# Optimization experiments

Measured on AMD Instinct MI355X. Metric: run time of the kernel, lower is better.

## Reference

```python
import jax, jax.numpy as jnp
import numpy as np

B, N, DS, DP, H, DH, DFF = 1, 1024, 768, 128, 16, 48, 1536


def _ln(x, eps=1e-5):
    m = jnp.mean(x, axis=-1, keepdims=True)
    v = jnp.var(x, axis=-1, keepdims=True)
    return (x - m) * jax.lax.rsqrt(v + eps)


def _ada_ln(a, s, gw, gb, bw):
    # AF3-style adaptive layernorm: sigmoid(Linear(LN(s))) * LN(a) + Linear(LN(s))
    sn = _ln(s)
    return jax.nn.sigmoid(sn @ gw + gb) * _ln(a) + sn @ bw


def setup_inputs() -> dict:
    key = jax.random.key(0)
    ks = jax.random.split(key, 24)
    w = lambda k, shape: jax.random.normal(k, shape, dtype=jnp.float32) * 0.02
    return {
        'x': jax.random.normal(ks[0], (B, N, DS), dtype=jnp.float32),
        'single_cond': jax.random.normal(ks[1], (B, N, DS), dtype=jnp.float32),
        'pair_cond': jax.random.normal(ks[2], (B, N, N, DP), dtype=jnp.float32),
        'attn_gamma_w': w(ks[3], (DS, DS)), 'attn_gamma_b': jnp.zeros((DS,), jnp.float32),
        'attn_beta_w': w(ks[4], (DS, DS)),
        'wq': w(ks[5], (DS, H * DH)), 'bq': jnp.zeros((H * DH,), jnp.float32),
        'wk': w(ks[6], (DS, H * DH)), 'wv': w(ks[7], (DS, H * DH)),
        'wb': w(ks[8], (DP, H)),
        'wg': w(ks[9], (DS, H * DH)),
        'wo': w(ks[10], (H * DH, DS)),
        'attn_gate_w': w(ks[11], (DS, DS)), 'attn_gate_b': jnp.full((DS,), -2.0, jnp.float32),
        'ff_gamma_w': w(ks[12], (DS, DS)), 'ff_gamma_b': jnp.zeros((DS,), jnp.float32),
        'ff_beta_w': w(ks[13], (DS, DS)),
        'ff_w1': w(ks[14], (DS, DFF)), 'ff_w2': w(ks[15], (DS, DFF)),
        'ff_w3': w(ks[16], (DFF, DS)),
        'ff_gate_w': w(ks[17], (DS, DS)), 'ff_gate_b': jnp.full((DS,), -2.0, jnp.float32),
        'mask': jnp.ones((B, N), dtype=bool),
    }


def reference(x, single_cond, pair_cond, attn_gamma_w, attn_gamma_b, attn_beta_w,
              wq, bq, wk, wv, wb, wg, wo, attn_gate_w, attn_gate_b,
              ff_gamma_w, ff_gamma_b, ff_beta_w, ff_w1, ff_w2, ff_w3,
              ff_gate_w, ff_gate_b, mask):
    # --- AttentionPairBias (edge bias + cond adaLN + gated output) ---
    a = _ada_ln(x, single_cond, attn_gamma_w, attn_gamma_b, attn_beta_w)
    q = (a @ wq + bq).reshape(B, N, H, DH)  # q has bias (q_use_bias=True)
    k = (a @ wk).reshape(B, N, H, DH)
    v = (a @ wv).reshape(B, N, H, DH)
    bias = jnp.einsum('bijp,ph->bhij', _ln(pair_cond), wb)  # pair bias per head
    logits = jnp.einsum('bihd,bjhd->bhij', q, k) * (1.0 / np.float32(np.sqrt(DH))) + bias
    logits = jnp.where(mask[:, None, None, :], logits, jnp.float32(-1e9))
    attn = jax.nn.softmax(logits, axis=-1)
    o = jnp.einsum('bhij,bjhd->bihd', attn, v)
    g = jax.nn.sigmoid(a @ wg).reshape(B, N, H, DH)  # gating (g_use_bias=False)
    attn_out = (g * o).reshape(B, N, H * DH) @ wo  # o_use_bias=False
    attn_out = jax.nn.sigmoid(single_cond @ attn_gate_w + attn_gate_b) * attn_out
    # --- ConditionedFeedForward (adaLN + SwiGLU + cond output gate) ---
    f = _ada_ln(x, single_cond, ff_gamma_w, ff_gamma_b, ff_beta_w)
    h = jax.nn.silu(f @ ff_w1) * (f @ ff_w2)
    ff_out = jax.nn.sigmoid(single_cond @ ff_gate_w + ff_gate_b) * (h @ ff_w3)
    # dropout p=0 (eval) -> identity; residual add of both branches
    return x + attn_out + ff_out
```

## Files before the change

### kernel.cpp

```cpp
#include <hip/hip_runtime.h>
#include <hip/hip_bf16.h>


typedef __attribute__((ext_vector_type(8))) short bf16x8;
typedef __attribute__((ext_vector_type(4))) float f32x4;
typedef __attribute__((ext_vector_type(4))) unsigned short us4;

#define DEVFN static __device__ __forceinline__

DEVFN float bf2f(unsigned short u){
  union { unsigned int u; float f; } v; v.u = ((unsigned int)u) << 16; return v.f;
}
DEVFN unsigned short f2bf(float f){
  union { float f; unsigned int u; } v; v.f = f;
  unsigned int r = v.u + 0x7fffu + ((v.u >> 16) & 1u);
  return (unsigned short)(r >> 16);
}
DEVFN float sigf(float x){ return 1.f / (1.f + __expf(-x)); }

DEVFN void gload16(const void* g, void* l){
  __builtin_amdgcn_global_load_lds(
      (const __attribute__((address_space(1))) void*)g,
      (__attribute__((address_space(3))) void*)l, 16, 0, 0);
}

#define OFF_SN    0x0000000ULL
#define OFF_SC    0x0180000ULL
#define OFF_XA    0x0300000ULL
#define OFF_W1    0x0600000ULL
#define OFF_W2    0x0A80000ULL
#define OFF_W3    0x0CC0000ULL
#define OFF_W4    0x1140000ULL
#define OFF_W5    0x15C0000ULL
#define OFF_W6    0x1800000ULL
#define OFF_BIAS1 0x1920000ULL
#define OFF_BIASG 0x1923000ULL
#define OFF_BIASQ 0x1924800ULL
#define OFF_G1    0x1930000ULL
#define OFF_GATES 0x2530000ULL
#define OFF_A     0x2B30000ULL
#define OFF_F     0x2CB0000ULL
#define OFF_QH    0x2E30000ULL
#define OFF_KH    0x2FB0000ULL
#define OFF_GH    0x3130000ULL
#define OFF_VT    0x3430000ULL
#define OFF_HH    0x4030000ULL
#define OFF_GO    0x4330000ULL
#define OFF_PB    0x47B0000ULL

struct WJobs {
  const float* src[14];
  unsigned long long dst[14];
  int K[14];
  int N[14];
  int rowmul[14];
  int rowoff[14];
};

__global__ __launch_bounds__(256) void prep_kernel(WJobs jobs, char* ws,
    const float* __restrict__ x, const float* __restrict__ sc,
    unsigned short* __restrict__ sn_bf, unsigned short* __restrict__ sc_bf,
    float* __restrict__ xa,
    const float* agb, const float* bq, const float* gtb, const float* fgtb,
    const float* fgb, float* bias1, float* biasg, float* biasq){
  const int bid = blockIdx.x;
  const int tid = threadIdx.x;
  if(bid < 9792){
    int t = bid, z = 0;
    while(true){
      int nt = (jobs.N[z] >> 5) * (jobs.K[z] >> 5);
      if(t < nt) break;
      t -= nt; z++;
    }
    const int nx = jobs.N[z] >> 5;
    const int n0 = (t % nx) << 5, k0 = (t / nx) << 5;
    const int K = jobs.K[z], N = jobs.N[z];
    __shared__ float tt[32][33];
    const int tx = tid & 31, ty = tid >> 5;
    const float* src = jobs.src[z];
    #pragma unroll
    for(int i=0;i<4;i++)
      tt[ty + i*8][tx] = src[(long long)(k0 + ty + i*8) * N + n0 + tx];
    __syncthreads();
    unsigned short* dst = (unsigned short*)(ws + jobs.dst[z]);
    const int rm = jobs.rowmul[z], ro = jobs.rowoff[z];
    #pragma unroll
    for(int i=0;i<4;i++)
      dst[(long long)((n0 + ty + i*8)*rm + ro) * K + k0 + tx] = f2bf(tt[tx][ty + i*8]);
    return;
  }
  if(bid >= 10816){
    int t = (bid - 10816) * 256 + tid;
    float v = 0.f;
    if(t < 768) v = agb[t];
    else if(t >= 1536 && t < 2304) v = fgb[t - 1536];
    bias1[t] = v;
    biasq[t] = (t < 768) ? bq[t] : 0.f;
    if(t < 1536) biasg[t] = (t < 768) ? gtb[t] : fgtb[t - 768];
    return;
  }
  const int row = bid - 9792;
  const float* xr = x + (long long)row * 768;
  const float* sr = sc + (long long)row * 768;
  float xs[3], ss[3];
  float s0=0.f, s1=0.f, s2=0.f, s3=0.f;
  #pragma unroll
  for(int i=0;i<3;i++){
    float xv = xr[tid + i*256], sv = sr[tid + i*256];
    xs[i]=xv; ss[i]=sv;
    s0 += xv; s1 += xv*xv; s2 += sv; s3 += sv*sv;
  }
  #pragma unroll
  for(int o=32;o;o>>=1){
    s0 += __shfl_xor(s0,o); s1 += __shfl_xor(s1,o);
    s2 += __shfl_xor(s2,o); s3 += __shfl_xor(s3,o);
  }
  __shared__ float red[4][4];
  const int w = tid >> 6;
  if((tid & 63) == 0){ red[0][w]=s0; red[1][w]=s1; red[2][w]=s2; red[3][w]=s3; }
  __syncthreads();
  float tx0 = red[0][0]+red[0][1]+red[0][2]+red[0][3];
  float tx1 = red[1][0]+red[1][1]+red[1][2]+red[1][3];
  float ts0 = red[2][0]+red[2][1]+red[2][2]+red[2][3];
  float ts1 = red[3][0]+red[3][1]+red[3][2]+red[3][3];
  const float inv = 1.f/768.f;
  float mx = tx0*inv, vx = tx1*inv - mx*mx;
  float ms = ts0*inv, vs = ts1*inv - ms*ms;
  float rsx = rsqrtf(vx + 1e-5f), rss = rsqrtf(vs + 1e-5f);
  #pragma unroll
  for(int i=0;i<3;i++){
    int c = tid + i*256;
    xa[(long long)row*768 + c]    = (xs[i]-mx)*rsx;
    sn_bf[(long long)row*768 + c] = f2bf((ss[i]-ms)*rss);
    sc_bf[(long long)row*768 + c] = f2bf(ss[i]);
  }
}

DEVFN void gemm_tile_f32(const unsigned short* __restrict__ A,
                         const unsigned short* __restrict__ Bt,
                         int N, int K, int m0, int n0,
                         const float* __restrict__ bias,
                         float* __restrict__ Cf, int epi,
                         unsigned short* sA, unsigned short* sB, int tid){
  const int w = tid >> 6, l = tid & 63, l15 = l & 15, l4 = l >> 4;
  const int wm = w >> 1, wn = w & 1;
  f32x4 zf = {0.f,0.f,0.f,0.f};
  f32x4 acc[4][4];
  #pragma unroll
  for(int m=0;m<4;m++)
    #pragma unroll
    for(int n=0;n<4;n++) acc[m][n] = zf;

  const int srow = w*16 + (l >> 2);
  const int scol = (l & 3) * 8;
  const unsigned short* gA = A  + (long long)(m0 + srow) * K + scol;
  const unsigned short* gB = Bt + (long long)(n0 + srow) * K + scol;
  unsigned short* lA0 = &sA[(w*16)*32];
  unsigned short* lA1 = &sA[(64 + w*16)*32];
  unsigned short* lB0 = &sB[(w*16)*32];
  unsigned short* lB1 = &sB[(64 + w*16)*32];
  const long long half = (long long)64 * K;

  for(int k0 = 0; k0 < K; k0 += 32){
    gload16(gA + k0, lA0);
    gload16(gA + half + k0, lA1);
    gload16(gB + k0, lB0);
    gload16(gB + half + k0, lB1);
    __syncthreads();
    bf16x8 af[4], bg[4];
    #pragma unroll
    for(int m=0;m<4;m++) af[m] = *(const bf16x8*)&sA[(wm*64 + m*16 + l15)*32 + l4*8];
    #pragma unroll
    for(int n=0;n<4;n++) bg[n] = *(const bf16x8*)&sB[(wn*64 + n*16 + l15)*32 + l4*8];
    #pragma unroll
    for(int m=0;m<4;m++)
      #pragma unroll
      for(int n=0;n<4;n++)
        acc[m][n] = __builtin_amdgcn_mfma_f32_16x16x32_bf16(af[m], bg[n], acc[m][n], 0, 0, 0);
    __syncthreads();
  }
  #pragma unroll
  for(int m=0;m<4;m++){
    #pragma unroll
    for(int n=0;n<4;n++){
      #pragma unroll
      for(int r=0;r<4;r++){
        const int i = m0 + wm*64 + m*16 + l4*4 + r;
        const int c = n0 + wn*64 + n*16 + l15;
        float v = acc[m][n][r] + bias[c];
        Cf[(long long)i*N + c] = epi ? sigf(v) : v;
      }
    }
  }
}

DEVFN void pair_block(int pbid, const float* __restrict__ pair,
                      const float* __restrict__ wb,
                      unsigned short* __restrict__ pb, int tid){
  const int l = tid & 63, w = tid >> 6, l15 = l & 15, l4 = l >> 4;
  bf16x8 wbf[4];
  #pragma unroll
  for(int c=0;c<4;c++){
    bf16x8 t;
    #pragma unroll
    for(int e=0;e<8;e++) t[e] = (short)f2bf(wb[(c*32 + l4*8 + e)*16 + l15]);
    wbf[c] = t;
  }
  f32x4 zf = {0.f,0.f,0.f,0.f};
  #pragma unroll
  for(int q=0;q<4;q++){
    const long long tile = (long long)pbid * 16 + q*4 + w;
    const long long row0 = tile << 4;
    const float* pr = pair + ((row0 + l15) << 7);
    float vals[32];
    #pragma unroll
    for(int c=0;c<4;c++){
      float4 v0 = *(const float4*)(pr + c*32 + l4*8);
      float4 v1 = *(const float4*)(pr + c*32 + l4*8 + 4);
      vals[c*8+0]=v0.x; vals[c*8+1]=v0.y; vals[c*8+2]=v0.z; vals[c*8+3]=v0.w;
      vals[c*8+4]=v1.x; vals[c*8+5]=v1.y; vals[c*8+6]=v1.z; vals[c*8+7]=v1.w;
    }
    float s=0.f, s2=0.f;
    #pragma unroll
    for(int e=0;e<32;e++){ s += vals[e]; s2 += vals[e]*vals[e]; }
    s += __shfl_xor(s, 16); s2 += __shfl_xor(s2, 16);
    s += __shfl_xor(s, 32); s2 += __shfl_xor(s2, 32);
    const float m = s * (1.f/128.f);
    const float rs = rsqrtf(s2*(1.f/128.f) - m*m + 1e-5f);
    f32x4 acc = zf;
    #pragma unroll
    for(int c=0;c<4;c++){
      bf16x8 af;
      #pragma unroll
      for(int e=0;e<8;e++) af[e] = (short)f2bf((vals[c*8+e] - m) * rs);
      acc = __builtin_amdgcn_mfma_f32_16x16x32_bf16(af, wbf[c], acc, 0,0,0);
    }
    us4 o;
    #pragma unroll
    for(int r=0;r<4;r++) o[r] = f2bf(acc[r]);
    *(us4*)&pb[((long long)l15 << 20) + row0 + l4*4] = o;
  }
}

__global__ __launch_bounds__(256) void fA_kernel(
    const float* __restrict__ pair, const float* __restrict__ wb,
    unsigned short* __restrict__ pb,
    const unsigned short* __restrict__ SN, const unsigned short* __restrict__ W1,
    const float* __restrict__ B1, float* __restrict__ G1,
    const unsigned short* __restrict__ SC, const unsigned short* __restrict__ W2,
    const float* __restrict__ BG, float* __restrict__ GT){
  __shared__ __align__(16) unsigned short sA[128*32];
  __shared__ __align__(16) unsigned short sB[128*32];
  const int bid = blockIdx.x;
  const int tid = threadIdx.x;
  if(bid < 288){
    if(bid < 192){
      gemm_tile_f32(SN, W1, 3072, 768, (bid & 7)*128, (bid >> 3)*128, B1, G1, 0, sA, sB, tid);
    } else {
      const int t = bid - 192;
      gemm_tile_f32(SC, W2, 1536, 768, (t & 7)*128, (t >> 3)*128, BG, GT, 1, sA, sB, tid);
    }
    return;
  }
  pair_block(bid - 288, pair, wb, pb, tid);
}

__global__ __launch_bounds__(256) void ew1_kernel(const float* __restrict__ g1,
    const float* __restrict__ xa, unsigned short* __restrict__ a_bf,
    unsigned short* __restrict__ f_bf, const float* __restrict__ x,
    float* __restrict__ out){
  const int i = blockIdx.x;
  const int c = blockIdx.y * 256 + threadIdx.x;
  const float* row = g1 + (long long)i * 3072;
  float xv = xa[(long long)i*768 + c];
  a_bf[(long long)i*768 + c] = f2bf(sigf(row[c])      * xv + row[768 + c]);
  f_bf[(long long)i*768 + c] = f2bf(sigf(row[1536+c]) * xv + row[2304 + c]);
  out[(long long)i*768 + c] = x[(long long)i*768 + c];
}

__global__ __launch_bounds__(256) void fB_kernel(
    const float* __restrict__ pair, const float* __restrict__ wb,
    unsigned short* __restrict__ pb,
    const unsigned short* __restrict__ A_, const unsigned short* __restrict__ W3,
    const float* __restrict__ BQ,
    unsigned short* __restrict__ QH, unsigned short* __restrict__ KH,
    unsigned short* __restrict__ GH, unsigned short* __restrict__ VT,
    const unsigned short* __restrict__ F_, const unsigned short* __restrict__ W4,
    unsigned short* __restrict__ HH){
  __shared__ __align__(16) unsigned short sA[128*32];
  __shared__ __align__(16) unsigned short sB[128*32];
  const int bid = blockIdx.x;
  const int tid = threadIdx.x;
  if(bid >= 384){
    pair_block(bid - 384 + 2048, pair, wb, pb, tid);
    return;
  }
  const bool isq = bid < 192;
  const int t = isq ? bid : bid - 192;
  const int m0 = (t & 7) * 128, n0 = (t >> 3) * 128;
  const unsigned short* A  = isq ? A_ : F_;
  const unsigned short* Bt = isq ? W3 : W4;
  const int K = 768;

  const int w = tid >> 6, l = tid & 63, l15 = l & 15, l4 = l >> 4;
  const int wm = w >> 1, wn = w & 1;
  f32x4 zf = {0.f,0.f,0.f,0.f};
  f32x4 acc[4][4];
  #pragma unroll
  for(int m=0;m<4;m++)
    #pragma unroll
    for(int n=0;n<4;n++) acc[m][n] = zf;

  const int srow = w*16 + (l >> 2);
  const int scol = (l & 3) * 8;
  const unsigned short* gA = A  + (long long)(m0 + srow) * K + scol;
  const unsigned short* gB = Bt + (long long)(n0 + srow) * K + scol;
  unsigned short* lA0 = &sA[(w*16)*32];
  unsigned short* lA1 = &sA[(64 + w*16)*32];
  unsigned short* lB0 = &sB[(w*16)*32];
  unsigned short* lB1 = &sB[(64 + w*16)*32];
  const long long half = (long long)64 * K;

  for(int k0 = 0; k0 < K; k0 += 32){
    gload16(gA + k0, lA0);
    gload16(gA + half + k0, lA1);
    gload16(gB + k0, lB0);
    gload16(gB + half + k0, lB1);
    __syncthreads();
    bf16x8 af[4], bg[4];
    #pragma unroll
    for(int m=0;m<4;m++) af[m] = *(const bf16x8*)&sA[(wm*64 + m*16 + l15)*32 + l4*8];
    #pragma unroll
    for(int n=0;n<4;n++) bg[n] = *(const bf16x8*)&sB[(wn*64 + n*16 + l15)*32 + l4*8];
    #pragma unroll
    for(int m=0;m<4;m++)
      #pragma unroll
      for(int n=0;n<4;n++)
        acc[m][n] = __builtin_amdgcn_mfma_f32_16x16x32_bf16(af[m], bg[n], acc[m][n], 0, 0, 0);
    __syncthreads();
  }
  if(isq){
    #pragma unroll
    for(int m=0;m<4;m++){
      #pragma unroll
      for(int n=0;n<4;n++){
        const int c = n0 + wn*64 + n*16 + l15;
        const int ibase = m0 + wm*64 + m*16 + l4*4;
        const int which = c / 768;
        const int h = (c % 768) / 48, d = c % 48;
        unsigned short vb[4];
        #pragma unroll
        for(int r=0;r<4;r++) vb[r] = f2bf(acc[m][n][r] + BQ[c]);
        if(which == 2){
          us4 o; o.x=vb[0]; o.y=vb[1]; o.z=vb[2]; o.w=vb[3];
          *(us4*)&VT[((long long)(c - 1536) << 10) + ibase] = o;
        } else {
          unsigned short* dst = (which == 0) ? QH : (which == 1) ? KH : GH;
          #pragma unroll
          for(int r=0;r<4;r++)
            dst[((long long)((h << 10) + ibase + r))*48 + d] = vb[r];
        }
      }
    }
  } else {
    #pragma unroll
    for(int m=0;m<4;m++){
      #pragma unroll
      for(int n=0;n<4;n++){
        #pragma unroll
        for(int r=0;r<4;r++){
          const int i = m0 + wm*64 + m*16 + l4*4 + r;
          const int c = n0 + wn*64 + n*16 + l15;
          float v = acc[m][n][r];
          float partner = __shfl_xor(v, 1);
          if((c & 1) == 0)
            HH[(long long)i*1536 + (c>>1)] = f2bf(v * sigf(v) * partner);
        }
      }
    }
  }
}

__global__ __launch_bounds__(256) void attn_kernel(
    const unsigned short* __restrict__ QH, const unsigned short* __restrict__ KH,
    const unsigned short* __restrict__ GH,
    const unsigned short* __restrict__ pbias,
    const unsigned short* __restrict__ VT,
    unsigned short* __restrict__ go){
  const int h  = blockIdx.x >> 6;
  const int i0 = (blockIdx.x & 63) << 4;
  const int tid = threadIdx.x;
  const int w = tid >> 6, l = tid & 63, l15 = l & 15, l4 = l >> 4;

  __shared__ unsigned short sP[16][1032];
  __shared__ float sRedM[16][4];
  __shared__ float sRedS[16][4];
  __shared__ float sO[4][16][48];

  f32x4 zf = {0.f,0.f,0.f,0.f};
  bf16x8 zero8 = {0,0,0,0,0,0,0,0};

  const unsigned short* pbh = pbias + ((long long)h << 20) + ((long long)i0 << 10);
  #pragma unroll
  for(int it=0; it<8; it++){
    const int idx = it*2048 + tid*8;
    const int r = idx >> 10, c = idx & 1023;
    *(bf16x8*)&sP[r][c] = *(const bf16x8*)&pbh[((long long)r << 10) + c];
  }

  f32x4 accs[16];
  #pragma unroll
  for(int f=0;f<16;f++) accs[f] = zf;
  bf16x8 aq0, aq1;
  {
    const unsigned short* qp = QH + (long long)((h << 10) + i0 + l15)*48;
    aq0 = *(const bf16x8*)(qp + l4*8);
    aq1 = *(const bf16x8*)(qp + 32 + l4*8);
  }
  const int jbase = w * 256;
  #pragma unroll
  for(int f=0; f<16; f++){
    const int j = jbase + f*16 + l15;
    const unsigned short* kp = KH + (long long)((h << 10) + j)*48;
    bf16x8 bk0 = *(const bf16x8*)(kp + l4*8);
    bf16x8 bk1 = *(const bf16x8*)(kp + 32 + l4*8);
    if(l4 >= 2) bk1 = zero8;
    accs[f] = __builtin_amdgcn_mfma_f32_16x16x32_bf16(aq0, bk0, accs[f], 0,0,0);
    accs[f] = __builtin_amdgcn_mfma_f32_16x16x32_bf16(aq1, bk1, accs[f], 0,0,0);
  }
  __syncthreads();

  const float scale = 0.14433756729740643f;
  #pragma unroll
  for(int f=0;f<16;f++){
    #pragma unroll
    for(int r=0;r<4;r++)
      accs[f][r] = accs[f][r]*scale + bf2f(sP[l4*4 + r][jbase + f*16 + l15]);
  }
  float pm[4];
  #pragma unroll
  for(int r=0;r<4;r++){
    float m = accs[0][r];
    #pragma unroll
    for(int f=1;f<16;f++) m = fmaxf(m, accs[f][r]);
    #pragma unroll
    for(int o=1;o<16;o<<=1) m = fmaxf(m, __shfl_xor(m, o));
    pm[r] = m;
  }
  if(l15 == 0){
    #pragma unroll
    for(int r=0;r<4;r++) sRedM[l4*4 + r][w] = pm[r];
  }
  __syncthreads();
  float rowm[4];
  #pragma unroll
  for(int r=0;r<4;r++){
    const int i = l4*4 + r;
    rowm[r] = fmaxf(fmaxf(sRedM[i][0], sRedM[i][1]), fmaxf(sRedM[i][2], sRedM[i][3]));
  }
  float psum[4] = {0.f,0.f,0.f,0.f};
  #pragma unroll
  for(int f=0;f<16;f++)
    #pragma unroll
    for(int r=0;r<4;r++){
      float p = __expf(accs[f][r] - rowm[r]);
      accs[f][r] = p;
      psum[r] += p;
    }
  #pragma unroll
  for(int r=0;r<4;r++)
    #pragma unroll
    for(int o=1;o<16;o<<=1) psum[r] += __shfl_xor(psum[r], o);
  if(l15 == 0){
    #pragma unroll
    for(int r=0;r<4;r++) sRedS[l4*4 + r][w] = psum[r];
  }
  #pragma unroll
  for(int f=0;f<16;f++)
    #pragma unroll
    for(int r=0;r<4;r++)
      sP[l4*4 + r][jbase + f*16 + l15] = f2bf(accs[f][r]);

  f32x4 acco[3];
  #pragma unroll
  for(int n=0;n<3;n++) acco[n] = zf;
  const unsigned short* vth = VT + ((long long)(h*48) << 10);
  #pragma unroll
  for(int c=0; c<4; c++){
    const int jb = jbase + c*64;
    #pragma unroll
    for(int kk=0; kk<2; kk++){
      bf16x8 pa = *(const bf16x8*)&sP[l15][jb + kk*32 + l4*8];
      #pragma unroll
      for(int n=0;n<3;n++){
        bf16x8 bv = *(const bf16x8*)&vth[((long long)(n*16 + l15) << 10) + jb + kk*32 + l4*8];
        acco[n] = __builtin_amdgcn_mfma_f32_16x16x32_bf16(pa, bv, acco[n], 0,0,0);
      }
    }
  }
  #pragma unroll
  for(int n=0;n<3;n++)
    #pragma unroll
    for(int r=0;r<4;r++)
      sO[w][l4*4 + r][n*16 + l15] = acco[n][r];
  __syncthreads();
  for(int t = tid; t < 768; t += 256){
    const int i = t / 48, d = t % 48;
    float o = sO[0][i][d] + sO[1][i][d] + sO[2][i][d] + sO[3][i][d];
    float lsum = sRedS[i][0] + sRedS[i][1] + sRedS[i][2] + sRedS[i][3];
    float gv = bf2f(GH[(long long)((h << 10) + i0 + i)*48 + d]);
    go[(long long)(i0 + i)*768 + h*48 + d] = f2bf(sigf(gv) * (o / lsum));
  }
}

__global__ __launch_bounds__(256) void final_kernel(
    const unsigned short* __restrict__ GO, const unsigned short* __restrict__ W6t,
    const unsigned short* __restrict__ HH, const unsigned short* __restrict__ W5t,
    const float* __restrict__ gates, float* __restrict__ out){
  __shared__ __align__(16) unsigned short sA[128*32];
  __shared__ __align__(16) unsigned short sB[128*32];
  const int m0 = blockIdx.x * 128, n0 = blockIdx.y * 128;
  const int z = blockIdx.z;
  const bool pA = z < 4;
  const unsigned short* A  = pA ? GO  : HH;
  const unsigned short* Bt = pA ? W6t : W5t;
  const int K    = pA ? 768 : 1536;
  const int kbeg = pA ? z*192 : (z-4)*384;
  const int kend = pA ? kbeg + 192 : kbeg + 384;
  const int goff = pA ? 0 : 768;
  const int tid = threadIdx.x;
  const int w = tid >> 6, l = tid & 63, l15 = l & 15, l4 = l >> 4;
  const int wm = w >> 1, wn = w & 1;
  f32x4 zf = {0.f,0.f,0.f,0.f};
  f32x4 acc[4][4];
  #pragma unroll
  for(int m=0;m<4;m++)
    #pragma unroll
    for(int n=0;n<4;n++) acc[m][n] = zf;

  const int srow = w*16 + (l >> 2);
  const int scol = (l & 3) * 8;
  const unsigned short* gA = A  + (long long)(m0 + srow) * K + scol;
  const unsigned short* gB = Bt + (long long)(n0 + srow) * K + scol;
  unsigned short* lA0 = &sA[(w*16)*32];
  unsigned short* lA1 = &sA[(64 + w*16)*32];
  unsigned short* lB0 = &sB[(w*16)*32];
  unsigned short* lB1 = &sB[(64 + w*16)*32];
  const long long half = (long long)64 * K;

  for(int k0 = kbeg; k0 < kend; k0 += 32){
    gload16(gA + k0, lA0);
    gload16(gA + half + k0, lA1);
    gload16(gB + k0, lB0);
    gload16(gB + half + k0, lB1);
    __syncthreads();
    bf16x8 af[4], bg[4];
    #pragma unroll
    for(int m=0;m<4;m++) af[m] = *(const bf16x8*)&sA[(wm*64 + m*16 + l15)*32 + l4*8];
    #pragma unroll
    for(int n=0;n<4;n++) bg[n] = *(const bf16x8*)&sB[(wn*64 + n*16 + l15)*32 + l4*8];
    #pragma unroll
    for(int m=0;m<4;m++)
      #pragma unroll
      for(int n=0;n<4;n++)
        acc[m][n] = __builtin_amdgcn_mfma_f32_16x16x32_bf16(af[m], bg[n], acc[m][n], 0, 0, 0);
    __syncthreads();
  }
  #pragma unroll
  for(int m=0;m<4;m++){
    #pragma unroll
    for(int n=0;n<4;n++){
      #pragma unroll
      for(int r=0;r<4;r++){
        const int i = m0 + wm*64 + m*16 + l4*4 + r;
        const int c = n0 + wn*64 + n*16 + l15;
        float v = gates[(long long)i*1536 + goff + c] * acc[m][n][r];
        __hip_atomic_fetch_add(&out[(long long)i*768 + c], v,
                               __ATOMIC_RELAXED, __HIP_MEMORY_SCOPE_AGENT);
      }
    }
  }
}

extern "C" void kernel_launch(void* const* d_in, const int* in_sizes, int n_in,
                              void* d_out, int out_size, void* d_ws, size_t ws_size,
                              hipStream_t stream){
  (void)in_sizes; (void)n_in; (void)out_size; (void)ws_size;
  const float* x    = (const float*)d_in[0];
  const float* sc   = (const float*)d_in[1];
  const float* pair = (const float*)d_in[2];
  const float* agw  = (const float*)d_in[3];
  const float* agb  = (const float*)d_in[4];
  const float* abw  = (const float*)d_in[5];
  const float* wq   = (const float*)d_in[6];
  const float* bq   = (const float*)d_in[7];
  const float* wk   = (const float*)d_in[8];
  const float* wv   = (const float*)d_in[9];
  const float* wb   = (const float*)d_in[10];
  const float* wg   = (const float*)d_in[11];
  const float* wo   = (const float*)d_in[12];
  const float* gtw  = (const float*)d_in[13];
  const float* gtb  = (const float*)d_in[14];
  const float* fgw  = (const float*)d_in[15];
  const float* fgb  = (const float*)d_in[16];
  const float* fbw  = (const float*)d_in[17];
  const float* fw1  = (const float*)d_in[18];
  const float* fw2  = (const float*)d_in[19];
  const float* fw3  = (const float*)d_in[20];
  const float* fgtw = (const float*)d_in[21];
  const float* fgtb = (const float*)d_in[22];
  float* out = (float*)d_out;
  char* ws = (char*)d_ws;

  unsigned short* SN   = (unsigned short*)(ws + OFF_SN);
  unsigned short* SC   = (unsigned short*)(ws + OFF_SC);
  float*          XA   = (float*)(ws + OFF_XA);
  unsigned short* W1   = (unsigned short*)(ws + OFF_W1);
  unsigned short* W2   = (unsigned short*)(ws + OFF_W2);
  unsigned short* W3   = (unsigned short*)(ws + OFF_W3);
  unsigned short* W4   = (unsigned short*)(ws + OFF_W4);
  unsigned short* W5   = (unsigned short*)(ws + OFF_W5);
  unsigned short* W6   = (unsigned short*)(ws + OFF_W6);
  float*          B1   = (float*)(ws + OFF_BIAS1);
  float*          BG   = (float*)(ws + OFF_BIASG);
  float*          BQ   = (float*)(ws + OFF_BIASQ);
  float*          G1   = (float*)(ws + OFF_G1);
  float*          GT   = (float*)(ws + OFF_GATES);
  unsigned short* A_   = (unsigned short*)(ws + OFF_A);
  unsigned short* F_   = (unsigned short*)(ws + OFF_F);
  unsigned short* QH   = (unsigned short*)(ws + OFF_QH);
  unsigned short* KH   = (unsigned short*)(ws + OFF_KH);
  unsigned short* GH   = (unsigned short*)(ws + OFF_GH);
  unsigned short* VT   = (unsigned short*)(ws + OFF_VT);
  unsigned short* HH   = (unsigned short*)(ws + OFF_HH);
  unsigned short* GO   = (unsigned short*)(ws + OFF_GO);
  unsigned short* PB   = (unsigned short*)(ws + OFF_PB);

  WJobs jobs;
  int ji = 0;
  auto setj = [&](const float* s, unsigned long long off, int K, int N,
                  int rm = 1, int ro = 0){
    jobs.src[ji]=s; jobs.dst[ji]=off; jobs.K[ji]=K; jobs.N[ji]=N;
    jobs.rowmul[ji]=rm; jobs.rowoff[ji]=ro; ji++;
  };
  const unsigned long long W768 = 768ULL*768ULL*2ULL;
  setj(agw,  OFF_W1 + 0*W768, 768, 768);
  setj(abw,  OFF_W1 + 1*W768, 768, 768);
  setj(fgw,  OFF_W1 + 2*W768, 768, 768);
  setj(fbw,  OFF_W1 + 3*W768, 768, 768);
  setj(gtw,  OFF_W2 + 0*W768, 768, 768);
  setj(fgtw, OFF_W2 + 1*W768, 768, 768);
  setj(wq,   OFF_W3 + 0*W768, 768, 768);
  setj(wk,   OFF_W3 + 1*W768, 768, 768);
  setj(wv,   OFF_W3 + 2*W768, 768, 768);
  setj(wg,   OFF_W3 + 3*W768, 768, 768);
  setj(fw1,  OFF_W4, 768, 1536, 2, 0);
  setj(fw2,  OFF_W4, 768, 1536, 2, 1);
  setj(fw3,  OFF_W5, 1536, 768);
  setj(wo,   OFF_W6, 768, 768);

  prep_kernel<<<10828, 256, 0, stream>>>(jobs, ws, x, sc, SN, SC, XA,
      agb, bq, gtb, fgtb, fgb, B1, BG, BQ);
  fA_kernel<<<2336, 256, 0, stream>>>(pair, wb, PB, SN, W1, B1, G1, SC, W2, BG, GT);
  ew1_kernel<<<dim3(1024,3), 256, 0, stream>>>(G1, XA, A_, F_, x, out);
  fB_kernel<<<2432, 256, 0, stream>>>(pair, wb, PB, A_, W3, BQ,
      QH, KH, GH, VT, F_, W4, HH);
  attn_kernel<<<1024, 256, 0, stream>>>(QH, KH, GH, PB, VT, GO);
  final_kernel<<<dim3(8,6,8), 256, 0, stream>>>(GO, W6, HH, W5, GT, out);
}
```

Before: 265.9 us.

## Fuse all stages into a persistent megakernel with grid barriers and pair-bias work stealing

Replaces the six separate kernel launches with one persistent kernel of 512 blocks that loops over the work items of each former kernel and separates stages with a software grid barrier built on atomics. The pair-bias LayerNorm-projection blocks become a dynamically drained queue, split across the first four stages so idle blocks fill gaps after the lighter stage work. The intent is to remove launch gaps and per-stage tail effects and to overlap the memory-bound pair-bias work with the GEMMs. Risks are the barrier cost, reliance on all 512 blocks being co-resident (launch bounds ask for 2 blocks per CU, with a timeout break as a fallback), the loss of __restrict__ hints, and register or LDS pressure from combining all stages in one kernel.

```diff
diff --git a/kernel.cpp b/kernel.cpp
--- a/kernel.cpp
+++ b/kernel.cpp
@@ -7,6 +7,7 @@
 typedef __attribute__((ext_vector_type(4))) unsigned short us4;
 
 #define DEVFN static __device__ __forceinline__
+#define NBLK 512
 
 DEVFN float bf2f(unsigned short u){
   union { unsigned int u; float f; } v; v.u = ((unsigned int)u) << 16; return v.f;
@@ -47,6 +48,7 @@
 #define OFF_HH    0x4030000ULL
 #define OFF_GO    0x4330000ULL
 #define OFF_PB    0x47B0000ULL
+#define OFF_SYNC  0x6800000ULL
 
 struct WJobs {
   const float* src[14];
@@ -57,40 +59,63 @@
   int rowoff[14];
 };
 
-__global__ __launch_bounds__(256) void prep_kernel(WJobs jobs, char* ws,
-    const float* __restrict__ x, const float* __restrict__ sc,
-    unsigned short* __restrict__ sn_bf, unsigned short* __restrict__ sc_bf,
-    float* __restrict__ xa,
+DEVFN void gridsync(unsigned* bar, unsigned* gen){
+  __syncthreads();
+  if(threadIdx.x == 0){
+    __threadfence();
+    unsigned g = __hip_atomic_load(gen, __ATOMIC_RELAXED, __HIP_MEMORY_SCOPE_AGENT);
+    unsigned a = __hip_atomic_fetch_add(bar, 1u, __ATOMIC_ACQ_REL, __HIP_MEMORY_SCOPE_AGENT);
+    if(a == (unsigned)(NBLK - 1)){
+      __hip_atomic_store(bar, 0u, __ATOMIC_RELAXED, __HIP_MEMORY_SCOPE_AGENT);
+      __hip_atomic_fetch_add(gen, 1u, __ATOMIC_RELEASE, __HIP_MEMORY_SCOPE_AGENT);
+    } else {
+      unsigned long long t0 = clock64();
+      while(__hip_atomic_load(gen, __ATOMIC_RELAXED, __HIP_MEMORY_SCOPE_AGENT) == g){
+        __builtin_amdgcn_s_sleep(8);
+        if(clock64() - t0 > 200000000ULL) break;
+      }
+    }
+    __threadfence();
+  }
+  __syncthreads();
+}
+
+DEVFN void transpose_tile(const WJobs& jobs, char* ws, int t, int tid, void* smem){
+  int z = 0;
+  while(true){
+    int nt = (jobs.N[z] >> 5) * (jobs.K[z] >> 5);
+    if(t < nt) break;
+    t -= nt; z++;
+  }
+  const int nx = jobs.N[z] >> 5;
+  const int n0 = (t % nx) << 5, k0 = (t / nx) << 5;
+  const int K = jobs.K[z], N = jobs.N[z];
+  float (*tt)[33] = (float(*)[33])smem;
+  const int tx = tid & 31, ty = tid >> 5;
+  const float* src = jobs.src[z];
+  #pragma unroll
+  for(int i=0;i<4;i++)
+    tt[ty + i*8][tx] = src[(long long)(k0 + ty + i*8) * N + n0 + tx];
+  __syncthreads();
+  unsigned short* dst = (unsigned short*)(ws + jobs.dst[z]);
+  const int rm = jobs.rowmul[z], ro = jobs.rowoff[z];
+  #pragma unroll
+  for(int i=0;i<4;i++)
+    dst[(long long)((n0 + ty + i*8)*rm + ro) * K + k0 + tx] = f2bf(tt[tx][ty + i*8]);
+  __syncthreads();
+}
+
+DEVFN void prep_item(const WJobs& jobs, char* ws, int it, int tid, void* smem,
+    const float* x, const float* sc,
+    unsigned short* sn_bf, unsigned short* sc_bf, float* xa,
     const float* agb, const float* bq, const float* gtb, const float* fgtb,
     const float* fgb, float* bias1, float* biasg, float* biasq){
-  const int bid = blockIdx.x;
-  const int tid = threadIdx.x;
-  if(bid < 9792){
-    int t = bid, z = 0;
-    while(true){
-      int nt = (jobs.N[z] >> 5) * (jobs.K[z] >> 5);
-      if(t < nt) break;
-      t -= nt; z++;
-    }
-    const int nx = jobs.N[z] >> 5;
-    const int n0 = (t % nx) << 5, k0 = (t / nx) << 5;
-    const int K = jobs.K[z], N = jobs.N[z];
-    __shared__ float tt[32][33];
-    const int tx = tid & 31, ty = tid >> 5;
-    const float* src = jobs.src[z];
-    #pragma unroll
-    for(int i=0;i<4;i++)
-      tt[ty + i*8][tx] = src[(long long)(k0 + ty + i*8) * N + n0 + tx];
-    __syncthreads();
-    unsigned short* dst = (unsigned short*)(ws + jobs.dst[z]);
-    const int rm = jobs.rowmul[z], ro = jobs.rowoff[z];
-    #pragma unroll
-    for(int i=0;i<4;i++)
-      dst[(long long)((n0 + ty + i*8)*rm + ro) * K + k0 + tx] = f2bf(tt[tx][ty + i*8]);
+  if(it < 9792){
+    transpose_tile(jobs, ws, it, tid, smem);
     return;
   }
-  if(bid >= 10816){
-    int t = (bid - 10816) * 256 + tid;
+  if(it >= 10816){
+    int t = (it - 10816) * 256 + tid;
     float v = 0.f;
     if(t < 768) v = agb[t];
     else if(t >= 1536 && t < 2304) v = fgb[t - 1536];
@@ -99,7 +124,7 @@
     if(t < 1536) biasg[t] = (t < 768) ? gtb[t] : fgtb[t - 768];
     return;
   }
-  const int row = bid - 9792;
+  const int row = it - 9792;
   const float* xr = x + (long long)row * 768;
   const float* sr = sc + (long long)row * 768;
   float xs[3], ss[3];
@@ -115,7 +140,7 @@
     s0 += __shfl_xor(s0,o); s1 += __shfl_xor(s1,o);
     s2 += __shfl_xor(s2,o); s3 += __shfl_xor(s3,o);
   }
-  __shared__ float red[4][4];
+  float (*red)[4] = (float(*)[4])smem;
   const int w = tid >> 6;
   if((tid & 63) == 0){ red[0][w]=s0; red[1][w]=s1; red[2][w]=s2; red[3][w]=s3; }
   __syncthreads();
@@ -134,13 +159,12 @@
     sn_bf[(long long)row*768 + c] = f2bf((ss[i]-ms)*rss);
     sc_bf[(long long)row*768 + c] = f2bf(ss[i]);
   }
-}
-
-DEVFN void gemm_tile_f32(const unsigned short* __restrict__ A,
-                         const unsigned short* __restrict__ Bt,
+  __syncthreads();
+}
+
+DEVFN void gemm_tile_f32(const unsigned short* A, const unsigned short* Bt,
                          int N, int K, int m0, int n0,
-                         const float* __restrict__ bias,
-                         float* __restrict__ Cf, int epi,
+                         const float* bias, float* Cf, int epi,
                          unsigned short* sA, unsigned short* sB, int tid){
   const int w = tid >> 6, l = tid & 63, l15 = l & 15, l4 = l >> 4;
   const int wm = w >> 1, wn = w & 1;
@@ -194,9 +218,8 @@
   }
 }
 
-DEVFN void pair_block(int pbid, const float* __restrict__ pair,
-                      const float* __restrict__ wb,
-                      unsigned short* __restrict__ pb, int tid){
+DEVFN void pair_block(int pbid, const float* pair, const float* wb,
+                      unsigned short* pb, int tid){
   const int l = tid & 63, w = tid >> 6, l15 = l & 15, l4 = l >> 4;
   bf16x8 wbf[4];
   #pragma unroll
@@ -242,35 +265,24 @@
   }
 }
 
-__global__ __launch_bounds__(256) void fA_kernel(
-    const float* __restrict__ pair, const float* __restrict__ wb,
-    unsigned short* __restrict__ pb,
-    const unsigned short* __restrict__ SN, const unsigned short* __restrict__ W1,
-    const float* __restrict__ B1, float* __restrict__ G1,
-    const unsigned short* __restrict__ SC, const unsigned short* __restrict__ W2,
-    const float* __restrict__ BG, float* __restrict__ GT){
-  __shared__ __align__(16) unsigned short sA[128*32];
-  __shared__ __align__(16) unsigned short sB[128*32];
-  const int bid = blockIdx.x;
-  const int tid = threadIdx.x;
-  if(bid < 288){
-    if(bid < 192){
-      gemm_tile_f32(SN, W1, 3072, 768, (bid & 7)*128, (bid >> 3)*128, B1, G1, 0, sA, sB, tid);
-    } else {
-      const int t = bid - 192;
-      gemm_tile_f32(SC, W2, 1536, 768, (t & 7)*128, (t >> 3)*128, BG, GT, 1, sA, sB, tid);
-    }
-    return;
-  }
-  pair_block(bid - 288, pair, wb, pb, tid);
-}
-
-__global__ __launch_bounds__(256) void ew1_kernel(const float* __restrict__ g1,
-    const float* __restrict__ xa, unsigned short* __restrict__ a_bf,
-    unsigned short* __restrict__ f_bf, const float* __restrict__ x,
-    float* __restrict__ out){
-  const int i = blockIdx.x;
-  const int c = blockIdx.y * 256 + threadIdx.x;
+DEVFN void pair_drain(unsigned* ctr, unsigned lo, unsigned hi,
+                      const float* pair, const float* wb,
+                      unsigned short* pb, int tid, volatile unsigned* qslot){
+  for(;;){
+    if(tid == 0)
+      *qslot = lo + __hip_atomic_fetch_add(ctr, 1u, __ATOMIC_RELAXED, __HIP_MEMORY_SCOPE_AGENT);
+    __syncthreads();
+    unsigned u = *qslot;
+    __syncthreads();
+    if(u >= hi) break;
+    pair_block((int)u, pair, wb, pb, tid);
+  }
+}
+
+DEVFN void ew1_item(int it, int tid, const float* g1, const float* xa,
+    unsigned short* a_bf, unsigned short* f_bf, const float* x, float* out){
+  const int i = it / 3;
+  const int c = (it % 3) * 256 + tid;
   const float* row = g1 + (long long)i * 3072;
   float xv = xa[(long long)i*768 + c];
   a_bf[(long long)i*768 + c] = f2bf(sigf(row[c])      * xv + row[768 + c]);
@@ -278,25 +290,12 @@
   out[(long long)i*768 + c] = x[(long long)i*768 + c];
 }
 
-__global__ __launch_bounds__(256) void fB_kernel(
-    const float* __restrict__ pair, const float* __restrict__ wb,
-    unsigned short* __restrict__ pb,
-    const unsigned short* __restrict__ A_, const unsigned short* __restrict__ W3,
-    const float* __restrict__ BQ,
-    unsigned short* __restrict__ QH, unsigned short* __restrict__ KH,
-    unsigned short* __restrict__ GH, unsigned short* __restrict__ VT,
-    const unsigned short* __restrict__ F_, const unsigned short* __restrict__ W4,
-    unsigned short* __restrict__ HH){
-  __shared__ __align__(16) unsigned short sA[128*32];
-  __shared__ __align__(16) unsigned short sB[128*32];
-  const int bid = blockIdx.x;
-  const int tid = threadIdx.x;
-  if(bid >= 384){
-    pair_block(bid - 384 + 2048, pair, wb, pb, tid);
-    return;
-  }
-  const bool isq = bid < 192;
-  const int t = isq ? bid : bid - 192;
+DEVFN void qkvg_hh_item(int it, int tid, unsigned short* sA, unsigned short* sB,
+    const unsigned short* A_, const unsigned short* W3, const float* BQ,
+    unsigned short* QH, unsigned short* KH, unsigned short* GH, unsigned short* VT,
+    const unsigned short* F_, const unsigned short* W4, unsigned short* HH){
+  const bool isq = it < 192;
+  const int t = isq ? it : it - 192;
   const int m0 = (t & 7) * 128, n0 = (t >> 3) * 128;
   const unsigned short* A  = isq ? A_ : F_;
   const unsigned short* Bt = isq ? W3 : W4;
@@ -381,29 +380,25 @@
   }
 }
 
-__global__ __launch_bounds__(256) void attn_kernel(
-    const unsigned short* __restrict__ QH, const unsigned short* __restrict__ KH,
-    const unsigned short* __restrict__ GH,
-    const unsigned short* __restrict__ pbias,
-    const unsigned short* __restrict__ VT,
-    unsigned short* __restrict__ go){
-  const int h  = blockIdx.x >> 6;
-  const int i0 = (blockIdx.x & 63) << 4;
-  const int tid = threadIdx.x;
+DEVFN void attn_item(int it, int tid, unsigned char* smem,
+    const unsigned short* QH, const unsigned short* KH, const unsigned short* GH,
+    const unsigned short* pbias, const unsigned short* VT, unsigned short* go){
+  const int h  = it >> 6;
+  const int i0 = (it & 63) << 4;
   const int w = tid >> 6, l = tid & 63, l15 = l & 15, l4 = l >> 4;
 
-  __shared__ unsigned short sP[16][1032];
-  __shared__ float sRedM[16][4];
-  __shared__ float sRedS[16][4];
-  __shared__ float sO[4][16][48];
+  unsigned short (*sP)[1032] = (unsigned short(*)[1032])smem;
+  float (*sRedM)[4] = (float(*)[4])(smem + 33024);
+  float (*sRedS)[4] = (float(*)[4])(smem + 33280);
+  float (*sO)[16][48] = (float(*)[16][48])(smem + 33536);
 
   f32x4 zf = {0.f,0.f,0.f,0.f};
   bf16x8 zero8 = {0,0,0,0,0,0,0,0};
 
   const unsigned short* pbh = pbias + ((long long)h << 20) + ((long long)i0 << 10);
   #pragma unroll
-  for(int it=0; it<8; it++){
-    const int idx = it*2048 + tid*8;
+  for(int itr=0; itr<8; itr++){
+    const int idx = itr*2048 + tid*8;
     const int r = idx >> 10, c = idx & 1023;
     *(bf16x8*)&sP[r][c] = *(const bf16x8*)&pbh[((long long)r << 10) + c];
   }
@@ -511,16 +506,15 @@
     float gv = bf2f(GH[(long long)((h << 10) + i0 + i)*48 + d]);
     go[(long long)(i0 + i)*768 + h*48 + d] = f2bf(sigf(gv) * (o / lsum));
   }
-}
-
-__global__ __launch_bounds__(256) void final_kernel(
-    const unsigned short* __restrict__ GO, const unsigned short* __restrict__ W6t,
-    const unsigned short* __restrict__ HH, const unsigned short* __restrict__ W5t,
-    const float* __restrict__ gates, float* __restrict__ out){
-  __shared__ __align__(16) unsigned short sA[128*32];
-  __shared__ __align__(16) unsigned short sB[128*32];
-  const int m0 = blockIdx.x * 128, n0 = blockIdx.y * 128;
-  const int z = blockIdx.z;
+  __syncthreads();
+}
+
+DEVFN void final_item(int it, int tid, unsigned short* sA, unsigned short* sB,
+    const unsigned short* GO, const unsigned short* W6t,
+    const unsigned short* HH, const unsigned short* W5t,
+    const float* gates, float* out){
+  const int z = it / 48, rem = it % 48;
+  const int m0 = (rem & 7) * 128, n0 = (rem >> 3) * 128;
   const bool pA = z < 4;
   const unsigned short* A  = pA ? GO  : HH;
   const unsigned short* Bt = pA ? W6t : W5t;
@@ -528,7 +522,6 @@
   const int kbeg = pA ? z*192 : (z-4)*384;
   const int kend = pA ? kbeg + 192 : kbeg + 384;
   const int goff = pA ? 0 : 768;
-  const int tid = threadIdx.x;
   const int w = tid >> 6, l = tid & 63, l15 = l & 15, l4 = l >> 4;
   const int wm = w >> 1, wn = w & 1;
   f32x4 zf = {0.f,0.f,0.f,0.f};
@@ -579,6 +572,88 @@
                                __ATOMIC_RELAXED, __HIP_MEMORY_SCOPE_AGENT);
       }
     }
+  }
+}
+
+__global__ void init_kernel(unsigned* sync){
+  if(threadIdx.x < 16) sync[threadIdx.x] = 0u;
+}
+
+__global__ __launch_bounds__(256, 2) void mega_kernel(
+    WJobs jobs, char* ws, unsigned* sync,
+    const float* x, const float* sc, const float* pair, const float* wb,
+    const float* agb, const float* bq, const float* gtb, const float* fgtb,
+    const float* fgb, float* out){
+  __shared__ __align__(16) unsigned char smem[46336];
+  const int bid = blockIdx.x, tid = threadIdx.x;
+  unsigned* bar  = sync + 0;
+  unsigned* gen  = sync + 1;
+  unsigned* pctr = sync + 2;
+  volatile unsigned* qslot = (volatile unsigned*)(smem + 46080);
+
+  unsigned short* SN = (unsigned short*)(ws + OFF_SN);
+  unsigned short* SC = (unsigned short*)(ws + OFF_SC);
+  float*          XA = (float*)(ws + OFF_XA);
+  unsigned short* W1 = (unsigned short*)(ws + OFF_W1);
+  unsigned short* W2 = (unsigned short*)(ws + OFF_W2);
+  unsigned short* W3 = (unsigned short*)(ws + OFF_W3);
+  unsigned short* W4 = (unsigned short*)(ws + OFF_W4);
+  unsigned short* W5 = (unsigned short*)(ws + OFF_W5);
+  unsigned short* W6 = (unsigned short*)(ws + OFF_W6);
+  float*          B1 = (float*)(ws + OFF_BIAS1);
+  float*          BG = (float*)(ws + OFF_BIASG);
+  float*          BQ = (float*)(ws + OFF_BIASQ);
+  float*          G1 = (float*)(ws + OFF_G1);
+  float*          GT = (float*)(ws + OFF_GATES);
+  unsigned short* A_ = (unsigned short*)(ws + OFF_A);
+  unsigned short* F_ = (unsigned short*)(ws + OFF_F);
+  unsigned short* QH = (unsigned short*)(ws + OFF_QH);
+  unsigned short* KH = (unsigned short*)(ws + OFF_KH);
+  unsigned short* GH = (unsigned short*)(ws + OFF_GH);
+  unsigned short* VT = (unsigned short*)(ws + OFF_VT);
+  unsigned short* HH = (unsigned short*)(ws + OFF_HH);
+  unsigned short* GO = (unsigned short*)(ws + OFF_GO);
+  unsigned short* PB = (unsigned short*)(ws + OFF_PB);
+  unsigned short* sA = (unsigned short*)smem;
+  unsigned short* sB = (unsigned short*)(smem + 8192);
+
+  for(int it = bid; it < 10828; it += NBLK)
+    prep_item(jobs, ws, it, tid, smem, x, sc, SN, SC, XA,
+              agb, bq, gtb, fgtb, fgb, B1, BG, BQ);
+  pair_drain(pctr+0, 0, 900, pair, wb, PB, tid, qslot);
+  gridsync(bar, gen);
+
+  for(int it = bid; it < 288; it += NBLK){
+    if(it < 192)
+      gemm_tile_f32(SN, W1, 3072, 768, (it & 7)*128, (it >> 3)*128, B1, G1, 0, sA, sB, tid);
+    else {
+      const int t = it - 192;
+      gemm_tile_f32(SC, W2, 1536, 768, (t & 7)*128, (t >> 3)*128, BG, GT, 1, sA, sB, tid);
+    }
+    __syncthreads();
+  }
+  pair_drain(pctr+1, 900, 1600, pair, wb, PB, tid, qslot);
+  gridsync(bar, gen);
+
+  for(int it = bid; it < 3072; it += NBLK)
+    ew1_item(it, tid, G1, XA, A_, F_, x, out);
+  pair_drain(pctr+2, 1600, 3000, pair, wb, PB, tid, qslot);
+  gridsync(bar, gen);
+
+  for(int it = bid; it < 384; it += NBLK){
+    qkvg_hh_item(it, tid, sA, sB, A_, W3, BQ, QH, KH, GH, VT, F_, W4, HH);
+    __syncthreads();
+  }
+  pair_drain(pctr+3, 3000, 4096, pair, wb, PB, tid, qslot);
+  gridsync(bar, gen);
+
+  for(int it = bid; it < 1024; it += NBLK)
+    attn_item(it, tid, smem, QH, KH, GH, PB, VT, GO);
+  gridsync(bar, gen);
+
+  for(int it = bid; it < 384; it += NBLK){
+    final_item(it, tid, sA, sB, GO, W6, HH, W5, GT, out);
+    __syncthreads();
   }
 }
 
@@ -612,30 +687,6 @@
   float* out = (float*)d_out;
   char* ws = (char*)d_ws;
 
-  unsigned short* SN   = (unsigned short*)(ws + OFF_SN);
-  unsigned short* SC   = (unsigned short*)(ws + OFF_SC);
-  float*          XA   = (float*)(ws + OFF_XA);
-  unsigned short* W1   = (unsigned short*)(ws + OFF_W1);
-  unsigned short* W2   = (unsigned short*)(ws + OFF_W2);
-  unsigned short* W3   = (unsigned short*)(ws + OFF_W3);
-  unsigned short* W4   = (unsigned short*)(ws + OFF_W4);
-  unsigned short* W5   = (unsigned short*)(ws + OFF_W5);
-  unsigned short* W6   = (unsigned short*)(ws + OFF_W6);
-  float*          B1   = (float*)(ws + OFF_BIAS1);
-  float*          BG   = (float*)(ws + OFF_BIASG);
-  float*          BQ   = (float*)(ws + OFF_BIASQ);
-  float*          G1   = (float*)(ws + OFF_G1);
-  float*          GT   = (float*)(ws + OFF_GATES);
-  unsigned short* A_   = (unsigned short*)(ws + OFF_A);
-  unsigned short* F_   = (unsigned short*)(ws + OFF_F);
-  unsigned short* QH   = (unsigned short*)(ws + OFF_QH);
-  unsigned short* KH   = (unsigned short*)(ws + OFF_KH);
-  unsigned short* GH   = (unsigned short*)(ws + OFF_GH);
-  unsigned short* VT   = (unsigned short*)(ws + OFF_VT);
-  unsigned short* HH   = (unsigned short*)(ws + OFF_HH);
-  unsigned short* GO   = (unsigned short*)(ws + OFF_GO);
-  unsigned short* PB   = (unsigned short*)(ws + OFF_PB);
-
   WJobs jobs;
   int ji = 0;
   auto setj = [&](const float* s, unsigned long long off, int K, int N,
@@ -659,12 +710,8 @@
   setj(fw3,  OFF_W5, 1536, 768);
   setj(wo,   OFF_W6, 768, 768);
 
-  prep_kernel<<<10828, 256, 0, stream>>>(jobs, ws, x, sc, SN, SC, XA,
-      agb, bq, gtb, fgtb, fgb, B1, BG, BQ);
-  fA_kernel<<<2336, 256, 0, stream>>>(pair, wb, PB, SN, W1, B1, G1, SC, W2, BG, GT);
-  ew1_kernel<<<dim3(1024,3), 256, 0, stream>>>(G1, XA, A_, F_, x, out);
-  fB_kernel<<<2432, 256, 0, stream>>>(pair, wb, PB, A_, W3, BQ,
-      QH, KH, GH, VT, F_, W4, HH);
-  attn_kernel<<<1024, 256, 0, stream>>>(QH, KH, GH, PB, VT, GO);
-  final_kernel<<<dim3(8,6,8), 256, 0, stream>>>(GO, W6, HH, W5, GT, out);
-}
+  unsigned* SYNC = (unsigned*)(ws + OFF_SYNC);
+  init_kernel<<<1, 64, 0, stream>>>(SYNC);
+  mega_kernel<<<NBLK, 256, 0, stream>>>(jobs, ws, SYNC,
+      x, sc, pair, wb, agb, bq, gtb, fgtb, fgb, out);
+}
```

Result: slower. 787.7 us (+196.3%).

## Move pair-bias LayerNorm projection into prep kernel, split GEMM kernels

Applied to the files above, without the earlier changes.

All 4096 pair-bias blocks now run inside the first (prep) launch, together with the weight transposes and row LayerNorms, instead of being spread across the two GEMM kernels. The GEMM kernels become plain 288- and 384-block launches. The intent is to let the bandwidth-bound pair streaming fill the GPU in one large launch while the GEMMs run without heterogeneous tail blocks. It also switches the pair LayerNorm bf16 conversion to truncation and sets an occupancy hint of 6 blocks on the merged kernel, which slightly changes rounding.

```diff
diff --git a/kernel.cpp b/kernel.cpp
--- a/kernel.cpp
+++ b/kernel.cpp
@@ -15,6 +15,10 @@
   union { float f; unsigned int u; } v; v.f = f;
   unsigned int r = v.u + 0x7fffu + ((v.u >> 16) & 1u);
   return (unsigned short)(r >> 16);
+}
+DEVFN unsigned short f2bf_trunc(float f){
+  union { float f; unsigned int u; } v; v.f = f;
+  return (unsigned short)(v.u >> 16);
 }
 DEVFN float sigf(float x){ return 1.f / (1.f + __expf(-x)); }
 
@@ -57,16 +61,70 @@
   int rowoff[14];
 };
 
-__global__ __launch_bounds__(256) void prep_kernel(WJobs jobs, char* ws,
+DEVFN void pair_block(int pbid, const float* __restrict__ pair,
+                      const float* __restrict__ wb,
+                      unsigned short* __restrict__ pb, int tid){
+  const int l = tid & 63, w = tid >> 6, l15 = l & 15, l4 = l >> 4;
+  bf16x8 wbf[4];
+  #pragma unroll
+  for(int c=0;c<4;c++){
+    bf16x8 t;
+    #pragma unroll
+    for(int e=0;e<8;e++) t[e] = (short)f2bf(wb[(c*32 + l4*8 + e)*16 + l15]);
+    wbf[c] = t;
+  }
+  #pragma unroll
+  for(int q=0;q<4;q++){
+    const long long row0 = (((long long)pbid) * 16 + q*4 + w) << 4;
+    const float* pr = pair + ((row0 + l15) << 7);
+    float vals[32];
+    #pragma unroll
+    for(int c=0;c<4;c++){
+      float4 v0 = *(const float4*)(pr + c*32 + l4*8);
+      float4 v1 = *(const float4*)(pr + c*32 + l4*8 + 4);
+      vals[c*8+0]=v0.x; vals[c*8+1]=v0.y; vals[c*8+2]=v0.z; vals[c*8+3]=v0.w;
+      vals[c*8+4]=v1.x; vals[c*8+5]=v1.y; vals[c*8+6]=v1.z; vals[c*8+7]=v1.w;
+    }
+    float s=0.f, s2=0.f;
+    #pragma unroll
+    for(int e=0;e<32;e++){ s += vals[e]; s2 += vals[e]*vals[e]; }
+    s += __shfl_xor(s, 16); s2 += __shfl_xor(s2, 16);
+    s += __shfl_xor(s, 32); s2 += __shfl_xor(s2, 32);
+    const float m = s * (1.f/128.f);
+    const float rs = rsqrtf(s2*(1.f/128.f) - m*m + 1e-5f);
+    f32x4 acc = {0.f,0.f,0.f,0.f};
+    #pragma unroll
+    for(int c=0;c<4;c++){
+      bf16x8 af;
+      #pragma unroll
+      for(int e=0;e<8;e++) af[e] = (short)f2bf_trunc((vals[c*8+e] - m) * rs);
+      acc = __builtin_amdgcn_mfma_f32_16x16x32_bf16(af, wbf[c], acc, 0,0,0);
+    }
+    us4 o;
+    #pragma unroll
+    for(int r=0;r<4;r++) o[r] = f2bf(acc[r]);
+    *(us4*)&pb[((long long)l15 << 20) + row0 + l4*4] = o;
+  }
+}
+
+__global__ __launch_bounds__(256, 6) void stream_kernel(WJobs jobs, char* ws,
+    const float* __restrict__ pair, const float* __restrict__ wb,
+    unsigned short* __restrict__ pb,
     const float* __restrict__ x, const float* __restrict__ sc,
     unsigned short* __restrict__ sn_bf, unsigned short* __restrict__ sc_bf,
     float* __restrict__ xa,
     const float* agb, const float* bq, const float* gtb, const float* fgtb,
     const float* fgb, float* bias1, float* biasg, float* biasq){
+  __shared__ __align__(16) float smem[32*33 + 16];
   const int bid = blockIdx.x;
   const int tid = threadIdx.x;
-  if(bid < 9792){
-    int t = bid, z = 0;
+  if(bid < 4096){
+    pair_block(bid, pair, wb, pb, tid);
+    return;
+  }
+  const int it = bid - 4096;
+  if(it < 9792){
+    int t = it, z = 0;
     while(true){
       int nt = (jobs.N[z] >> 5) * (jobs.K[z] >> 5);
       if(t < nt) break;
@@ -75,7 +133,7 @@
     const int nx = jobs.N[z] >> 5;
     const int n0 = (t % nx) << 5, k0 = (t / nx) << 5;
     const int K = jobs.K[z], N = jobs.N[z];
-    __shared__ float tt[32][33];
+    float (*tt)[33] = (float(*)[33])smem;
     const int tx = tid & 31, ty = tid >> 5;
     const float* src = jobs.src[z];
     #pragma unroll
@@ -89,8 +147,8 @@
       dst[(long long)((n0 + ty + i*8)*rm + ro) * K + k0 + tx] = f2bf(tt[tx][ty + i*8]);
     return;
   }
-  if(bid >= 10816){
-    int t = (bid - 10816) * 256 + tid;
+  if(it >= 10816){
+    int t = (it - 10816) * 256 + tid;
     float v = 0.f;
     if(t < 768) v = agb[t];
     else if(t >= 1536 && t < 2304) v = fgb[t - 1536];
@@ -99,7 +157,7 @@
     if(t < 1536) biasg[t] = (t < 768) ? gtb[t] : fgtb[t - 768];
     return;
   }
-  const int row = bid - 9792;
+  const int row = it - 9792;
   const float* xr = x + (long long)row * 768;
   const float* sr = sc + (long long)row * 768;
   float xs[3], ss[3];
@@ -115,7 +173,7 @@
     s0 += __shfl_xor(s0,o); s1 += __shfl_xor(s1,o);
     s2 += __shfl_xor(s2,o); s3 += __shfl_xor(s3,o);
   }
-  __shared__ float red[4][4];
+  float (*red)[4] = (float(*)[4])smem;
   const int w = tid >> 6;
   if((tid & 63) == 0){ red[0][w]=s0; red[1][w]=s1; red[2][w]=s2; red[3][w]=s3; }
   __syncthreads();
@@ -194,57 +252,7 @@
   }
 }
 
-DEVFN void pair_block(int pbid, const float* __restrict__ pair,
-                      const float* __restrict__ wb,
-                      unsigned short* __restrict__ pb, int tid){
-  const int l = tid & 63, w = tid >> 6, l15 = l & 15, l4 = l >> 4;
-  bf16x8 wbf[4];
-  #pragma unroll
-  for(int c=0;c<4;c++){
-    bf16x8 t;
-    #pragma unroll
-    for(int e=0;e<8;e++) t[e] = (short)f2bf(wb[(c*32 + l4*8 + e)*16 + l15]);
-    wbf[c] = t;
-  }
-  f32x4 zf = {0.f,0.f,0.f,0.f};
-  #pragma unroll
-  for(int q=0;q<4;q++){
-    const long long tile = (long long)pbid * 16 + q*4 + w;
-    const long long row0 = tile << 4;
-    const float* pr = pair + ((row0 + l15) << 7);
-    float vals[32];
-    #pragma unroll
-    for(int c=0;c<4;c++){
-      float4 v0 = *(const float4*)(pr + c*32 + l4*8);
-      float4 v1 = *(const float4*)(pr + c*32 + l4*8 + 4);
-      vals[c*8+0]=v0.x; vals[c*8+1]=v0.y; vals[c*8+2]=v0.z; vals[c*8+3]=v0.w;
-      vals[c*8+4]=v1.x; vals[c*8+5]=v1.y; vals[c*8+6]=v1.z; vals[c*8+7]=v1.w;
-    }
-    float s=0.f, s2=0.f;
-    #pragma unroll
-    for(int e=0;e<32;e++){ s += vals[e]; s2 += vals[e]*vals[e]; }
-    s += __shfl_xor(s, 16); s2 += __shfl_xor(s2, 16);
-    s += __shfl_xor(s, 32); s2 += __shfl_xor(s2, 32);
-    const float m = s * (1.f/128.f);
-    const float rs = rsqrtf(s2*(1.f/128.f) - m*m + 1e-5f);
-    f32x4 acc = zf;
-    #pragma unroll
-    for(int c=0;c<4;c++){
-      bf16x8 af;
-      #pragma unroll
-      for(int e=0;e<8;e++) af[e] = (short)f2bf((vals[c*8+e] - m) * rs);
-      acc = __builtin_amdgcn_mfma_f32_16x16x32_bf16(af, wbf[c], acc, 0,0,0);
-    }
-    us4 o;
-    #pragma unroll
-    for(int r=0;r<4;r++) o[r] = f2bf(acc[r]);
-    *(us4*)&pb[((long long)l15 << 20) + row0 + l4*4] = o;
-  }
-}
-
-__global__ __launch_bounds__(256) void fA_kernel(
-    const float* __restrict__ pair, const float* __restrict__ wb,
-    unsigned short* __restrict__ pb,
+__global__ __launch_bounds__(256) void gemmA_kernel(
     const unsigned short* __restrict__ SN, const unsigned short* __restrict__ W1,
     const float* __restrict__ B1, float* __restrict__ G1,
     const unsigned short* __restrict__ SC, const unsigned short* __restrict__ W2,
@@ -253,16 +261,12 @@
   __shared__ __align__(16) unsigned short sB[128*32];
   const int bid = blockIdx.x;
   const int tid = threadIdx.x;
-  if(bid < 288){
-    if(bid < 192){
-      gemm_tile_f32(SN, W1, 3072, 768, (bid & 7)*128, (bid >> 3)*128, B1, G1, 0, sA, sB, tid);
-    } else {
-      const int t = bid - 192;
-      gemm_tile_f32(SC, W2, 1536, 768, (t & 7)*128, (t >> 3)*128, BG, GT, 1, sA, sB, tid);
-    }
-    return;
-  }
-  pair_block(bid - 288, pair, wb, pb, tid);
+  if(bid < 192){
+    gemm_tile_f32(SN, W1, 3072, 768, (bid & 7)*128, (bid >> 3)*128, B1, G1, 0, sA, sB, tid);
+  } else {
+    const int t = bid - 192;
+    gemm_tile_f32(SC, W2, 1536, 768, (t & 7)*128, (t >> 3)*128, BG, GT, 1, sA, sB, tid);
+  }
 }
 
 __global__ __launch_bounds__(256) void ew1_kernel(const float* __restrict__ g1,
@@ -278,9 +282,7 @@
   out[(long long)i*768 + c] = x[(long long)i*768 + c];
 }
 
-__global__ __launch_bounds__(256) void fB_kernel(
-    const float* __restrict__ pair, const float* __restrict__ wb,
-    unsigned short* __restrict__ pb,
+__global__ __launch_bounds__(256) void gemmB_kernel(
     const unsigned short* __restrict__ A_, const unsigned short* __restrict__ W3,
     const float* __restrict__ BQ,
     unsigned short* __restrict__ QH, unsigned short* __restrict__ KH,
@@ -291,10 +293,6 @@
   __shared__ __align__(16) unsigned short sB[128*32];
   const int bid = blockIdx.x;
   const int tid = threadIdx.x;
-  if(bid >= 384){
-    pair_block(bid - 384 + 2048, pair, wb, pb, tid);
-    return;
-  }
   const bool isq = bid < 192;
   const int t = isq ? bid : bid - 192;
   const int m0 = (t & 7) * 128, n0 = (t >> 3) * 128;
@@ -659,12 +657,11 @@
   setj(fw3,  OFF_W5, 1536, 768);
   setj(wo,   OFF_W6, 768, 768);
 
-  prep_kernel<<<10828, 256, 0, stream>>>(jobs, ws, x, sc, SN, SC, XA,
-      agb, bq, gtb, fgtb, fgb, B1, BG, BQ);
-  fA_kernel<<<2336, 256, 0, stream>>>(pair, wb, PB, SN, W1, B1, G1, SC, W2, BG, GT);
+  stream_kernel<<<14924, 256, 0, stream>>>(jobs, ws, pair, wb, PB,
+      x, sc, SN, SC, XA, agb, bq, gtb, fgtb, fgb, B1, BG, BQ);
+  gemmA_kernel<<<288, 256, 0, stream>>>(SN, W1, B1, G1, SC, W2, BG, GT);
   ew1_kernel<<<dim3(1024,3), 256, 0, stream>>>(G1, XA, A_, F_, x, out);
-  fB_kernel<<<2432, 256, 0, stream>>>(pair, wb, PB, A_, W3, BQ,
-      QH, KH, GH, VT, F_, W4, HH);
+  gemmB_kernel<<<384, 256, 0, stream>>>(A_, W3, BQ, QH, KH, GH, VT, F_, W4, HH);
   attn_kernel<<<1024, 256, 0, stream>>>(QH, KH, GH, PB, VT, GO);
   final_kernel<<<dim3(8,6,8), 256, 0, stream>>>(GO, W6, HH, W5, GT, out);
 }
```

After: 305.1 us. 1.15x slower.
